# Performance work log

Measured on AMD Instinct MI355X. Metric: run time of the kernel, lower is better.

## Reference

```python
import jax, jax.numpy as jnp
import numpy as np

B, IN, H = 4096, 2048, 2048


def setup_inputs() -> dict:
    key = jax.random.key(0)
    ks = jax.random.split(key, 20)
    s_in = 1.0 / np.sqrt(IN)
    s_h = 1.0 / np.sqrt(H)
    inp = {
        "x": jax.random.normal(ks[0], (B, IN), jnp.float32),
        "h": jax.random.normal(ks[1], (B, H), jnp.float32),
        "c": jax.random.normal(ks[2], (B, H), jnp.float32),
    }
    names_in = [("Wii", "bii"), ("Wif", "bif"), ("Wig", "big"), ("Wio", "bio")]
    names_h = [("Whi", "bhi"), ("Whf", "bhf"), ("Whg", "bhg"), ("Who", "bho")]
    k = 3
    for wn, bn in names_in:
        inp[wn] = jax.random.normal(ks[k], (H, IN), jnp.float32) * s_in
        inp[bn] = jax.random.normal(ks[k + 1], (H,), jnp.float32) * s_in
        k += 2
    for wn, bn in names_h:
        inp[wn] = jax.random.normal(ks[k], (H, H), jnp.float32) * s_h
        inp[bn] = jax.random.normal(ks[k + 1], (H,), jnp.float32) * s_h
        k += 2
    return inp


def reference(x, h, c, Wii, bii, Whi, bhi, Wif, bif, Whf, bhf,
              Wig, big, Whg, bhg, Wio, bio, Who, bho):
    # Fuse the 4 input-projections and 4 hidden-projections into two GEMMs
    # (same math as 8 separate nn.Linear calls).
    Wx = jnp.concatenate([Wii, Wif, Wig, Wio], axis=0)   # [4H, IN]
    Wh = jnp.concatenate([Whi, Whf, Whg, Who], axis=0)   # [4H, H]
    bx = jnp.concatenate([bii, bif, big, bio])            # [4H]
    bh = jnp.concatenate([bhi, bhf, bhg, bho])            # [4H]
    gates = x @ Wx.T + h @ Wh.T + bx + bh                 # [B, 4H]
    ii, ff, gg, oo = jnp.split(gates, 4, axis=-1)
    i = jax.nn.sigmoid(ii)
    f = jax.nn.sigmoid(ff)
    g = jnp.tanh(gg)
    o = jax.nn.sigmoid(oo)
    c_new = f * c + i * g
    h_new = o * jnp.tanh(c_new)
    return jnp.stack([h_new, c_new])  # [2, B, H]
```

## Files before the change

### kernel.cpp

```cpp
#include <hip/hip_runtime.h>
#include <stdint.h>

typedef __attribute__((ext_vector_type(4))) float f32x4;
typedef __attribute__((ext_vector_type(8))) short bf16x8;

#define MFMA_BF16 __builtin_amdgcn_mfma_f32_16x16x32_bf16

__device__ __forceinline__ unsigned short f2bf(float f) {
  union { float f; uint32_t u; } a; a.f = f;
  uint32_t u = a.u;
  uint32_t r = (u + 0x7FFFu + ((u >> 16) & 1u)) >> 16;
  return (unsigned short)r;
}

__global__ void pack_all_kernel(const float4* __restrict__ x, const float4* __restrict__ hh,
                                const float* __restrict__ Wii, const float* __restrict__ Wif,
                                const float* __restrict__ Wig, const float* __restrict__ Wio,
                                const float* __restrict__ Whi, const float* __restrict__ Whf,
                                const float* __restrict__ Whg, const float* __restrict__ Who,
                                ushort4* __restrict__ A, ushort4* __restrict__ Wp) {
  const int total = 12582912;
  for (int q = blockIdx.x * blockDim.x + threadIdx.x; q < total; q += gridDim.x * blockDim.x) {
    if (q < 4194304) {
      int row = q >> 10, cq = q & 1023;
      float4 v = (cq < 512) ? x[row * 512 + cq] : hh[row * 512 + (cq - 512)];
      ushort4 o; o.x = f2bf(v.x); o.y = f2bf(v.y); o.z = f2bf(v.z); o.w = f2bf(v.w);
      A[q] = o;
    } else {
      int wq = q - 4194304;
      int p = wq >> 10, kq = wq & 1023;
      int r = p & 255;
      int g = ((r >> 7) << 1) | ((r >> 4) & 1);
      int H = ((p >> 8) << 6) | (((r >> 5) & 3) << 4) | (r & 15);
      const float* src;
      if (kq < 512) src = (g == 0) ? Wii : (g == 1) ? Wif : (g == 2) ? Wig : Wio;
      else          src = (g == 0) ? Whi : (g == 1) ? Whf : (g == 2) ? Whg : Who;
      const float4 v = *(const float4*)&src[(size_t)H * 2048 + ((kq & 511) << 2)];
      ushort4 o; o.x = f2bf(v.x); o.y = f2bf(v.y); o.z = f2bf(v.z); o.w = f2bf(v.w);
      Wp[wq] = o;
    }
  }
}

#define BAR __builtin_amdgcn_s_barrier()
#define LGKM0 asm volatile("s_waitcnt lgkmcnt(0)" ::: "memory")

#define STGH(srcH, kOff, dstE)                                                  \
  __builtin_amdgcn_global_load_lds(                                             \
      (const __attribute__((address_space(1))) void*)((srcH) + (kOff)),         \
      (__attribute__((address_space(3))) void*)(&smem[dstE]), 16, 0, 0);        \
  __builtin_amdgcn_global_load_lds(                                             \
      (const __attribute__((address_space(1))) void*)((srcH) + 32768 + (kOff)), \
      (__attribute__((address_space(3))) void*)(&smem[(dstE) + 512]), 16, 0, 0)

#define TILE8(bufE_, nbufE_, kA1_, kT2_, ST_A1, ST_T2, ENDM)                       \
  {                                                                                \
    bf16x8 af0[4][2], af1[4][2], b01[2][2], b23[2][2];                             \
                      \
    _Pragma("unroll") for (int m = 0; m < 4; ++m) {                                \
      af0[m][0] = *(const bf16x8*)&smem[(bufE_) + aR + m * 1024 + colE0];          \
      af0[m][1] = *(const bf16x8*)&smem[(bufE_) + aR + m * 1024 + colE1];          \
    }                                                                              \
    _Pragma("unroll") for (int n = 0; n < 2; ++n) {                                \
      b01[n][0] = *(const bf16x8*)&smem[(bufE_) + 16384 + bR + n * 1024 + colE0];  \
      b01[n][1] = *(const bf16x8*)&smem[(bufE_) + 16384 + bR + n * 1024 + colE1];  \
    }                                                                              \
    if (ST_A1) { STGH(aSrcH1, kA1_, (nbufE_) + 8192 + dstW); }                     \
    asm volatile("s_waitcnt lgkmcnt(8)" ::: "memory");                             \
    BAR; LGKM0;                                                                    \
    __builtin_amdgcn_s_setprio(1);                                                 \
    _Pragma("unroll") for (int m = 0; m < 4; ++m)                                  \
      _Pragma("unroll") for (int n = 0; n < 2; ++n) {                              \
        acc[m][n] = MFMA_BF16(af0[m][0], b01[n][0], acc[m][n], 0, 0, 0);           \
        acc[m][n] = MFMA_BF16(af0[m][1], b01[n][1], acc[m][n], 0, 0, 0);           \
      }                                                                            \
    __builtin_amdgcn_s_setprio(0);                                                 \
    BAR;                                                                           \
                            \
    _Pragma("unroll") for (int n = 0; n < 2; ++n) {                                \
      b23[n][0] = *(const bf16x8*)&smem[(bufE_) + 24576 + bR + n * 1024 + colE0];  \
      b23[n][1] = *(const bf16x8*)&smem[(bufE_) + 24576 + bR + n * 1024 + colE1];  \
    }                                                                              \
    if (ST_T2) { STGH(aSrcH0, kT2_, (bufE_) + dstW); }                             \
    BAR; LGKM0;                                                                    \
    __builtin_amdgcn_s_setprio(1);                                                 \
    _Pragma("unroll") for (int m = 0; m < 4; ++m)                                  \
      _Pragma("unroll") for (int n = 0; n < 2; ++n) {                              \
        acc[m][2 + n] = MFMA_BF16(af0[m][0], b23[n][0], acc[m][2 + n], 0, 0, 0);   \
        acc[m][2 + n] = MFMA_BF16(af0[m][1], b23[n][1], acc[m][2 + n], 0, 0, 0);   \
      }                                                                            \
    __builtin_amdgcn_s_setprio(0);                                                 \
    BAR;                                                                           \
                            \
    _Pragma("unroll") for (int m = 0; m < 4; ++m) {                                \
      af1[m][0] = *(const bf16x8*)&smem[(bufE_) + 8192 + aR + m * 1024 + colE0];   \
      af1[m][1] = *(const bf16x8*)&smem[(bufE_) + 8192 + aR + m * 1024 + colE1];   \
    }                                                                              \
    if (ST_T2) { STGH(bSrcH0, kT2_, (bufE_) + 16384 + dstW); }                     \
    BAR; LGKM0;                                                                    \
    __builtin_amdgcn_s_setprio(1);                                                 \
    _Pragma("unroll") for (int m = 0; m < 4; ++m)                                  \
      _Pragma("unroll") for (int n = 0; n < 2; ++n) {                              \
        acc[4 + m][n] = MFMA_BF16(af1[m][0], b01[n][0], acc[4 + m][n], 0, 0, 0);   \
        acc[4 + m][n] = MFMA_BF16(af1[m][1], b01[n][1], acc[4 + m][n], 0, 0, 0);   \
      }                                                                            \
    __builtin_amdgcn_s_setprio(0);                                                 \
    BAR;                                                                           \
                 \
    if (ST_T2) { STGH(bSrcH1, kT2_, (bufE_) + 24576 + dstW); }                     \
    BAR;                                                                           \
    __builtin_amdgcn_s_setprio(1);                                                 \
    _Pragma("unroll") for (int m = 0; m < 4; ++m)                                  \
      _Pragma("unroll") for (int n = 0; n < 2; ++n) {                              \
        acc[4 + m][2 + n] = MFMA_BF16(af1[m][0], b23[n][0], acc[4 + m][2 + n], 0, 0, 0); \
        acc[4 + m][2 + n] = MFMA_BF16(af1[m][1], b23[n][1], acc[4 + m][2 + n], 0, 0, 0); \
      }                                                                            \
    __builtin_amdgcn_s_setprio(0);                                                 \
    if ((ENDM) == 0) { asm volatile("s_waitcnt vmcnt(6)" ::: "memory"); BAR; }     \
    else if ((ENDM) == 1) { asm volatile("s_waitcnt vmcnt(0)" ::: "memory"); BAR; } \
  }

__global__ __launch_bounds__(512, 2)
void lstm_gemm_kernel(const ushort* __restrict__ A, const ushort* __restrict__ Wp,
                      const float* __restrict__ c,
                      const float* __restrict__ bii, const float* __restrict__ bif_,
                      const float* __restrict__ big_, const float* __restrict__ bio_,
                      const float* __restrict__ bhi, const float* __restrict__ bhf,
                      const float* __restrict__ bhg, const float* __restrict__ bho,
                      float* __restrict__ out) {
  __shared__ ushort smem[65536];
  const int tid = threadIdx.x;
  const int lane = tid & 63, w = tid >> 6;
  const int wm = w >> 2, wn = w & 3;

  const int bid = blockIdx.x;
  const int xcd = bid & 7, qq = bid >> 3;
  const int bn = (xcd << 2) | (qq >> 4);
  const int bm = qq & 15;

  const int laneRow = lane & 15, lane16 = lane >> 4;
  const int lr7 = laneRow & 7;
  const int colE0 = (lane16 ^ lr7) << 3;
  const int colE1 = ((4 + lane16) ^ lr7) << 3;

  const int chunkOff = ((lane & 7) ^ (lane >> 3)) << 3;
  const ushort* aSrcH0 = A + (size_t)(bm * 256 + 16 * w + (lane >> 3)) * 4096 + chunkOff;
  const ushort* aSrcH1 = aSrcH0 + (size_t)128 * 4096;
  const ushort* bSrcH0 = Wp + (size_t)(bn * 256 + 16 * w + (lane >> 3)) * 4096 + chunkOff;
  const ushort* bSrcH1 = bSrcH0 + (size_t)128 * 4096;
  const int dstW = w * 1024;

  const int aR = (wm * 64 + laneRow) * 64;
  const int bR = (wn * 32 + laneRow) * 64;

  f32x4 acc[8][4];
#pragma unroll
  for (int i = 0; i < 8; i++)
#pragma unroll
    for (int j = 0; j < 4; j++) acc[i][j] = (f32x4){0.f, 0.f, 0.f, 0.f};

  STGH(aSrcH0, 0, dstW);
  STGH(bSrcH0, 0, 16384 + dstW);
  STGH(bSrcH1, 0, 24576 + dstW);
  STGH(aSrcH1, 0, 8192 + dstW);
  STGH(aSrcH0, 64, 32768 + dstW);
  STGH(bSrcH0, 64, 32768 + 16384 + dstW);
  STGH(bSrcH1, 64, 32768 + 24576 + dstW);
  asm volatile("s_waitcnt vmcnt(6)" ::: "memory");
  BAR;

#pragma unroll 1
  for (int T = 0; T < 62; T += 2) {
    const int kA = (T + 1) << 6, kB = (T + 2) << 6, kC = (T + 3) << 6;
    TILE8(0, 32768, kA, kB, true, true, 0);
    TILE8(32768, 0, kB, kC, true, true, 0);
  }
  TILE8(0, 32768, 63 << 6, 0, true, false, 1);
  TILE8(32768, 0, 0, 0, false, false, 2);

  const int hcol = bn * 64 + wn * 16 + laneRow;
  const float bI = bii[hcol] + bhi[hcol];
  const float bF = bif_[hcol] + bhf[hcol];
  const float bG = big_[hcol] + bhg[hcol];
  const float bO = bio_[hcol] + bho[hcol];
#pragma unroll
  for (int mi = 0; mi < 8; ++mi) {
    const int rowBase = bm * 256 + (mi >> 2) * 128 + wm * 64 + (mi & 3) * 16 + lane16 * 4;
#pragma unroll
    for (int rr = 0; rr < 4; ++rr) {
      const int row = rowBase + rr;
      const float ii = acc[mi][0][rr] + bI;
      const float ff = acc[mi][1][rr] + bF;
      const float gg = acc[mi][2][rr] + bG;
      const float oo = acc[mi][3][rr] + bO;
      const float iv = 1.f / (1.f + __expf(-ii));
      const float fv = 1.f / (1.f + __expf(-ff));
      const float gv = tanhf(gg);
      const float ov = 1.f / (1.f + __expf(-oo));
      const float cv = c[(size_t)row * 2048 + hcol];
      const float cn = fv * cv + iv * gv;
      const float hn = ov * tanhf(cn);
      out[(size_t)row * 2048 + hcol] = hn;
      out[(size_t)8388608 + (size_t)row * 2048 + hcol] = cn;
    }
  }
}

extern "C" void kernel_launch(void* const* d_in, const int* in_sizes, int n_in,
                              void* d_out, int out_size, void* d_ws, size_t ws_size,
                              hipStream_t stream) {
  const float* x = (const float*)d_in[0];
  const float* h = (const float*)d_in[1];
  const float* c = (const float*)d_in[2];
  const float* Wii = (const float*)d_in[3];  const float* bii = (const float*)d_in[4];
  const float* Wif = (const float*)d_in[5];  const float* bif_ = (const float*)d_in[6];
  const float* Wig = (const float*)d_in[7];  const float* big_ = (const float*)d_in[8];
  const float* Wio = (const float*)d_in[9];  const float* bio_ = (const float*)d_in[10];
  const float* Whi = (const float*)d_in[11]; const float* bhi = (const float*)d_in[12];
  const float* Whf = (const float*)d_in[13]; const float* bhf = (const float*)d_in[14];
  const float* Whg = (const float*)d_in[15]; const float* bhg = (const float*)d_in[16];
  const float* Who = (const float*)d_in[17]; const float* bho = (const float*)d_in[18];

  ushort* Abf = (ushort*)d_ws;
  ushort* Wpk = Abf + (size_t)4096 * 4096;
  float* out = (float*)d_out;

  pack_all_kernel<<<3072, 256, 0, stream>>>((const float4*)x, (const float4*)h,
                                            Wii, Wif, Wig, Wio, Whi, Whf, Whg, Who,
                                            (ushort4*)Abf, (ushort4*)Wpk);
  lstm_gemm_kernel<<<512, 512, 0, stream>>>(Abf, Wpk, c,
                                            bii, bif_, big_, bio_, bhi, bhf, bhg, bho, out);
}
```

Baseline: 312.7 us.

## Cut per-tile barriers and move the vmcnt wait to the start of each GEMM tile

Restructures the double-buffered bf16 MFMA main loop so each K tile uses three workgroup barriers instead of about six, and drops the explicit lgkmcnt(0) waits. The global-to-LDS prefetches for the A0 and B0 sub-tiles are grouped into one slot. The vmcnt wait now sits at the top of each tile instead of the bottom, and the prologue barrier is removed. MFMA issue order changes to put the k-half loop outermost. The aim is less barrier stalling between waves and better overlap of LDS reads and global prefetch with MFMA, at the cost of tighter reasoning about LDS buffer reuse hazards.

```diff
diff --git a/kernel.cpp b/kernel.cpp
--- a/kernel.cpp
+++ b/kernel.cpp
@@ -42,8 +42,7 @@
   }
 }
 
-#define BAR __builtin_amdgcn_s_barrier()
-#define LGKM0 asm volatile("s_waitcnt lgkmcnt(0)" ::: "memory")
+#define BARF asm volatile("s_barrier" ::: "memory")
 
 #define STGH(srcH, kOff, dstE)                                                  \
   __builtin_amdgcn_global_load_lds(                                             \
@@ -53,71 +52,56 @@
       (const __attribute__((address_space(1))) void*)((srcH) + 32768 + (kOff)), \
       (__attribute__((address_space(3))) void*)(&smem[(dstE) + 512]), 16, 0, 0)
 
-#define TILE8(bufE_, nbufE_, kA1_, kT2_, ST_A1, ST_T2, ENDM)                       \
-  {                                                                                \
-    bf16x8 af0[4][2], af1[4][2], b01[2][2], b23[2][2];                             \
-                      \
-    _Pragma("unroll") for (int m = 0; m < 4; ++m) {                                \
-      af0[m][0] = *(const bf16x8*)&smem[(bufE_) + aR + m * 1024 + colE0];          \
-      af0[m][1] = *(const bf16x8*)&smem[(bufE_) + aR + m * 1024 + colE1];          \
-    }                                                                              \
-    _Pragma("unroll") for (int n = 0; n < 2; ++n) {                                \
-      b01[n][0] = *(const bf16x8*)&smem[(bufE_) + 16384 + bR + n * 1024 + colE0];  \
-      b01[n][1] = *(const bf16x8*)&smem[(bufE_) + 16384 + bR + n * 1024 + colE1];  \
-    }                                                                              \
-    if (ST_A1) { STGH(aSrcH1, kA1_, (nbufE_) + 8192 + dstW); }                     \
-    asm volatile("s_waitcnt lgkmcnt(8)" ::: "memory");                             \
-    BAR; LGKM0;                                                                    \
-    __builtin_amdgcn_s_setprio(1);                                                 \
-    _Pragma("unroll") for (int m = 0; m < 4; ++m)                                  \
-      _Pragma("unroll") for (int n = 0; n < 2; ++n) {                              \
-        acc[m][n] = MFMA_BF16(af0[m][0], b01[n][0], acc[m][n], 0, 0, 0);           \
-        acc[m][n] = MFMA_BF16(af0[m][1], b01[n][1], acc[m][n], 0, 0, 0);           \
-      }                                                                            \
-    __builtin_amdgcn_s_setprio(0);                                                 \
-    BAR;                                                                           \
-                            \
-    _Pragma("unroll") for (int n = 0; n < 2; ++n) {                                \
-      b23[n][0] = *(const bf16x8*)&smem[(bufE_) + 24576 + bR + n * 1024 + colE0];  \
-      b23[n][1] = *(const bf16x8*)&smem[(bufE_) + 24576 + bR + n * 1024 + colE1];  \
-    }                                                                              \
-    if (ST_T2) { STGH(aSrcH0, kT2_, (bufE_) + dstW); }                             \
-    BAR; LGKM0;                                                                    \
-    __builtin_amdgcn_s_setprio(1);                                                 \
-    _Pragma("unroll") for (int m = 0; m < 4; ++m)                                  \
-      _Pragma("unroll") for (int n = 0; n < 2; ++n) {                              \
-        acc[m][2 + n] = MFMA_BF16(af0[m][0], b23[n][0], acc[m][2 + n], 0, 0, 0);   \
-        acc[m][2 + n] = MFMA_BF16(af0[m][1], b23[n][1], acc[m][2 + n], 0, 0, 0);   \
-      }                                                                            \
-    __builtin_amdgcn_s_setprio(0);                                                 \
-    BAR;                                                                           \
-                            \
-    _Pragma("unroll") for (int m = 0; m < 4; ++m) {                                \
-      af1[m][0] = *(const bf16x8*)&smem[(bufE_) + 8192 + aR + m * 1024 + colE0];   \
-      af1[m][1] = *(const bf16x8*)&smem[(bufE_) + 8192 + aR + m * 1024 + colE1];   \
-    }                                                                              \
-    if (ST_T2) { STGH(bSrcH0, kT2_, (bufE_) + 16384 + dstW); }                     \
-    BAR; LGKM0;                                                                    \
-    __builtin_amdgcn_s_setprio(1);                                                 \
-    _Pragma("unroll") for (int m = 0; m < 4; ++m)                                  \
-      _Pragma("unroll") for (int n = 0; n < 2; ++n) {                              \
-        acc[4 + m][n] = MFMA_BF16(af1[m][0], b01[n][0], acc[4 + m][n], 0, 0, 0);   \
-        acc[4 + m][n] = MFMA_BF16(af1[m][1], b01[n][1], acc[4 + m][n], 0, 0, 0);   \
-      }                                                                            \
-    __builtin_amdgcn_s_setprio(0);                                                 \
-    BAR;                                                                           \
-                 \
-    if (ST_T2) { STGH(bSrcH1, kT2_, (bufE_) + 24576 + dstW); }                     \
-    BAR;                                                                           \
-    __builtin_amdgcn_s_setprio(1);                                                 \
-    _Pragma("unroll") for (int m = 0; m < 4; ++m)                                  \
-      _Pragma("unroll") for (int n = 0; n < 2; ++n) {                              \
-        acc[4 + m][2 + n] = MFMA_BF16(af1[m][0], b23[n][0], acc[4 + m][2 + n], 0, 0, 0); \
-        acc[4 + m][2 + n] = MFMA_BF16(af1[m][1], b23[n][1], acc[4 + m][2 + n], 0, 0, 0); \
-      }                                                                            \
-    __builtin_amdgcn_s_setprio(0);                                                 \
-    if ((ENDM) == 0) { asm volatile("s_waitcnt vmcnt(6)" ::: "memory"); BAR; }     \
-    else if ((ENDM) == 1) { asm volatile("s_waitcnt vmcnt(0)" ::: "memory"); BAR; } \
+#define Q(ACCR, ACCC, AF_, BF_)                                                 \
+  _Pragma("unroll") for (int kk = 0; kk < 2; ++kk)                              \
+    _Pragma("unroll") for (int m = 0; m < 4; ++m)                               \
+      _Pragma("unroll") for (int n = 0; n < 2; ++n)                             \
+        acc[(ACCR) + m][(ACCC) + n] =                                           \
+            MFMA_BF16(AF_[m][kk], BF_[n][kk], acc[(ACCR) + m][(ACCC) + n], 0, 0, 0);
+
+#define TILE(bufE_, nbufE_, kA1_, kT2_, ST_A1, ST_T2, VMC)                       \
+  {                                                                              \
+    if ((VMC) == 6) asm volatile("s_waitcnt vmcnt(6)" ::: "memory");             \
+    else            asm volatile("s_waitcnt vmcnt(0)" ::: "memory");             \
+    BARF;                              \
+    bf16x8 af0[4][2], af1[4][2], b01[2][2], b23[2][2];                           \
+                                                                        \
+    _Pragma("unroll") for (int m = 0; m < 4; ++m) {                              \
+      af0[m][0] = *(const bf16x8*)&smem[(bufE_) + aR + m * 1024 + colE0];        \
+      af0[m][1] = *(const bf16x8*)&smem[(bufE_) + aR + m * 1024 + colE1];        \
+    }                                                                            \
+    _Pragma("unroll") for (int n = 0; n < 2; ++n) {                              \
+      b01[n][0] = *(const bf16x8*)&smem[(bufE_) + 16384 + bR + n * 1024 + colE0];\
+      b01[n][1] = *(const bf16x8*)&smem[(bufE_) + 16384 + bR + n * 1024 + colE1];\
+    }                                                                            \
+    if (ST_A1) { STGH(aSrcH1, kA1_, (nbufE_) + 8192 + dstW); }                   \
+    __builtin_amdgcn_s_setprio(1);                                               \
+    Q(0, 0, af0, b01);                                                           \
+    __builtin_amdgcn_s_setprio(0);                                               \
+    BARF;                \
+                                                                        \
+    _Pragma("unroll") for (int n = 0; n < 2; ++n) {                              \
+      b23[n][0] = *(const bf16x8*)&smem[(bufE_) + 24576 + bR + n * 1024 + colE0];\
+      b23[n][1] = *(const bf16x8*)&smem[(bufE_) + 24576 + bR + n * 1024 + colE1];\
+    }                                                                            \
+    if (ST_T2) {                                                                 \
+      STGH(aSrcH0, kT2_, (bufE_) + dstW);                                        \
+      STGH(bSrcH0, kT2_, (bufE_) + 16384 + dstW);                                \
+    }                                                                            \
+    __builtin_amdgcn_s_setprio(1);                                               \
+    Q(0, 2, af0, b23);                                                           \
+    __builtin_amdgcn_s_setprio(0);                                               \
+    BARF;                              \
+                                                                        \
+    _Pragma("unroll") for (int m = 0; m < 4; ++m) {                              \
+      af1[m][0] = *(const bf16x8*)&smem[(bufE_) + 8192 + aR + m * 1024 + colE0]; \
+      af1[m][1] = *(const bf16x8*)&smem[(bufE_) + 8192 + aR + m * 1024 + colE1]; \
+    }                                                                            \
+    if (ST_T2) { STGH(bSrcH1, kT2_, (bufE_) + 24576 + dstW); }                   \
+    __builtin_amdgcn_s_setprio(1);                                               \
+    Q(4, 0, af1, b01);                                                           \
+    Q(4, 2, af1, b23);                                                           \
+    __builtin_amdgcn_s_setprio(0);                                               \
   }
 
 __global__ __launch_bounds__(512, 2)
@@ -166,17 +150,15 @@
   STGH(aSrcH0, 64, 32768 + dstW);
   STGH(bSrcH0, 64, 32768 + 16384 + dstW);
   STGH(bSrcH1, 64, 32768 + 24576 + dstW);
-  asm volatile("s_waitcnt vmcnt(6)" ::: "memory");
-  BAR;
 
 #pragma unroll 1
   for (int T = 0; T < 62; T += 2) {
     const int kA = (T + 1) << 6, kB = (T + 2) << 6, kC = (T + 3) << 6;
-    TILE8(0, 32768, kA, kB, true, true, 0);
-    TILE8(32768, 0, kB, kC, true, true, 0);
-  }
-  TILE8(0, 32768, 63 << 6, 0, true, false, 1);
-  TILE8(32768, 0, 0, 0, false, false, 2);
+    TILE(0, 32768, kA, kB, true, true, 6);
+    TILE(32768, 0, kB, kC, true, true, 6);
+  }
+  TILE(0, 32768, 63 << 6, 0, true, false, 6);
+  TILE(32768, 0, 0, 0, false, false, 0);
 
   const int hcol = bn * 64 + wn * 16 + laneRow;
   const float bI = bii[hcol] + bhi[hcol];
```

Measured after the change: 305.1 us. 2.4% less time.
